# Kernel optimization log

Measured on AMD Instinct MI355X. Metric: run time of the kernel, lower is better.

Reference implementation:

```python
import jax, jax.numpy as jnp
import numpy as np

N_NODES = 100000
N_EDGES = 1600000
N_GRAPHS = 128
CONV = [64, 64, 64]
HID = [256, 128, 2]
GFT = 64
EPS = 1e-5
NEG_SLOPE = 0.01


def leaky_relu(x):
    return jnp.where(x >= 0, x, NEG_SLOPE * x)


def setup_inputs() -> dict:
    key = jax.random.key(0)
    ks = jax.random.split(key, 32)
    inp = {}
    inp['x'] = jax.random.normal(ks[0], (N_NODES, CONV[0]), dtype=jnp.float32)
    inp['edge_index'] = jax.random.randint(ks[1], (2, N_EDGES), 0, N_NODES, dtype=jnp.int64)
    inp['graph_features'] = jax.random.normal(ks[2], (N_GRAPHS, GFT), dtype=jnp.float32)
    inp['batch'] = jnp.sort(jax.random.randint(ks[3], (N_NODES,), 0, N_GRAPHS, dtype=jnp.int64))
    # SAGEConv params per layer: W_l (aggregated branch, with bias), W_r (root branch), BN gamma/beta
    ki = 4
    for li in range(len(CONV) - 1):
        fin, fout = CONV[li], CONV[li + 1]
        s = 1.0 / np.sqrt(fin)
        inp[f'Wl{li}'] = jax.random.uniform(ks[ki], (fin, fout), minval=-s, maxval=s); ki += 1
        inp[f'bl{li}'] = jax.random.uniform(ks[ki], (fout,), minval=-s, maxval=s); ki += 1
        inp[f'Wr{li}'] = jax.random.uniform(ks[ki], (fin, fout), minval=-s, maxval=s); ki += 1
        inp[f'g{li}'] = jnp.ones((fout,), jnp.float32)
        inp[f'b{li}'] = jnp.zeros((fout,), jnp.float32)
    # MLP: Linear(128->256), LeakyReLU, Linear(256->128), LeakyReLU, Linear(128->2)
    dims = [CONV[-1] + GFT] + HID
    for li in range(len(HID)):
        fin, fout = dims[li], dims[li + 1]
        s = 1.0 / np.sqrt(fin)
        inp[f'Wm{li}'] = jax.random.uniform(ks[ki], (fin, fout), minval=-s, maxval=s); ki += 1
        inp[f'bm{li}'] = jax.random.uniform(ks[ki], (fout,), minval=-s, maxval=s); ki += 1
    return inp


def _sage_block(x, src, dst, Wl, bl, Wr, gamma, beta):
    # PyG SAGEConv (aggr='mean'): out = lin_l(mean_{j in N(i)} x_j) + lin_r(x_i)
    msgs = x[src]                                               # [E, Fin] gather
    agg = jax.ops.segment_sum(msgs, dst, num_segments=N_NODES)  # [N, Fin] scatter-add
    deg = jax.ops.segment_sum(jnp.ones((src.shape[0],), x.dtype), dst, num_segments=N_NODES)
    agg = agg / jnp.maximum(deg, 1.0)[:, None]
    h = agg @ Wl + bl + x @ Wr
    h = leaky_relu(h)
    # BatchNorm1d (training mode: batch stats over nodes, biased variance)
    mu = h.mean(axis=0)
    var = h.var(axis=0)
    return (h - mu) * jax.lax.rsqrt(var + EPS) * gamma + beta


def reference(x, edge_index, graph_features, batch,
              Wl0, bl0, Wr0, g0, b0, Wl1, bl1, Wr1, g1, b1,
              Wm0, bm0, Wm1, bm1, Wm2, bm2):
    src, dst = edge_index[0], edge_index[1]
    h = _sage_block(x, src, dst, Wl0, bl0, Wr0, g0, b0)
    h = _sage_block(h, src, dst, Wl1, bl1, Wr1, g1, b1)
    # scatter_mean graph pooling
    pooled = jax.ops.segment_sum(h, batch, num_segments=N_GRAPHS)
    cnt = jax.ops.segment_sum(jnp.ones((h.shape[0],), h.dtype), batch, num_segments=N_GRAPHS)
    pooled = pooled / jnp.maximum(cnt, 1.0)[:, None]
    z = jnp.concatenate([pooled, graph_features], axis=1)       # [G, 128]
    z = leaky_relu(z @ Wm0 + bm0)
    z = leaky_relu(z @ Wm1 + bm1)
    return z @ Wm2 + bm2
```

## Files before the change

kernel.cpp:

```cpp
#include <hip/hip_runtime.h>

#define N_NODES 100000
#define N_EDGES 1600000
#define N_GRAPHS 128
#define FDIM 64
#define EPSV 1e-5f
#define NEG 0.01f

#define NB 782
#define PART_BLOCKS 391
#define NTILES 6250
#define TPB 8
#define GEMM_BLOCKS 782

typedef short bf16x8 __attribute__((ext_vector_type(8)));
typedef float f32x4  __attribute__((ext_vector_type(4)));

__device__ __forceinline__ float leaky(float x){ return x >= 0.f ? x : NEG*x; }

__device__ __forceinline__ unsigned short f2bf(float x){
    unsigned u = __float_as_uint(x);
    return (unsigned short)((u + 0x7fffu + ((u >> 16) & 1u)) >> 16);
}
__device__ __forceinline__ float bf2f(unsigned short b){
    return __uint_as_float(((unsigned)b) << 16);
}

__device__ __forceinline__ void split8(const float4& v0, const float4& v1,
                                       bf16x8& hi, bf16x8& lo){
    float f[8] = {v0.x, v0.y, v0.z, v0.w, v1.x, v1.y, v1.z, v1.w};
    #pragma unroll
    for (int i = 0; i < 8; ++i){
        unsigned u = __float_as_uint(f[i]);
        hi[i] = (short)(u >> 16);
        float lf = f[i] - __uint_as_float(u & 0xffff0000u);
        lo[i] = (short)(__float_as_uint(lf) >> 16);
    }
}

__global__ __launch_bounds__(256) void k_cvt(const float* __restrict__ x,
                                             unsigned short* __restrict__ o){
    int i = blockIdx.x*256 + threadIdx.x;
    if (i < (N_NODES*FDIM)/4){
        float4 v = ((const float4*)x)[i];
        ushort4 r;
        r.x = f2bf(v.x); r.y = f2bf(v.y); r.z = f2bf(v.z); r.w = f2bf(v.w);
        ((ushort4*)o)[i] = r;
    }
}

__global__ __launch_bounds__(256) void k_bh(const int* __restrict__ dst, int* __restrict__ bhist){
    __shared__ int lh[NB];
    int t = threadIdx.x;
    for (int i = t; i < NB; i += 256) lh[i] = 0;
    __syncthreads();
    int base = blockIdx.x * 4096;
    #pragma unroll
    for (int k = 0; k < 16; ++k){
        int e = base + k*256 + t;
        if (e < N_EDGES) atomicAdd(&lh[dst[e] >> 7], 1);
    }
    __syncthreads();
    for (int i = t; i < NB; i += 256) if (lh[i]) atomicAdd(&bhist[i], lh[i]);
}

__global__ __launch_bounds__(256) void k_bscan(const int* __restrict__ bhist,
                                               int* __restrict__ boff, int* __restrict__ cur){
    __shared__ int lds[256];
    int t = threadIdx.x;
    int base = t*4;
    int v0 = (base+0 < NB) ? bhist[base+0] : 0;
    int v1 = (base+1 < NB) ? bhist[base+1] : 0;
    int v2 = (base+2 < NB) ? bhist[base+2] : 0;
    int v3 = (base+3 < NB) ? bhist[base+3] : 0;
    lds[t] = v0+v1+v2+v3; __syncthreads();
    for (int off = 1; off < 256; off <<= 1){
        int add = (t >= off) ? lds[t-off] : 0; __syncthreads();
        lds[t] += add; __syncthreads();
    }
    int excl = (t > 0) ? lds[t-1] : 0;
    int p0 = excl, p1 = excl+v0, p2 = excl+v0+v1, p3 = excl+v0+v1+v2;
    if (base+0 < NB){ boff[base+0] = p0; cur[base+0] = p0; }
    if (base+1 < NB){ boff[base+1] = p1; cur[base+1] = p1; }
    if (base+2 < NB){ boff[base+2] = p2; cur[base+2] = p2; }
    if (base+3 < NB){ boff[base+3] = p3; cur[base+3] = p3; }
    if (t == 0) boff[NB] = N_EDGES;
}

__global__ __launch_bounds__(256) void k_part(const int* __restrict__ src, const int* __restrict__ dst,
                                              int* __restrict__ cur, int* __restrict__ packed){
    __shared__ int lh[NB];
    __shared__ int lc[NB];
    int t = threadIdx.x;
    for (int i = t; i < NB; i += 256) lh[i] = 0;
    __syncthreads();
    int base = blockIdx.x * 4096;
    int d[16];
    #pragma unroll
    for (int k = 0; k < 16; ++k){
        int e = base + k*256 + t;
        d[k] = (e < N_EDGES) ? dst[e] : -1;
        if (d[k] >= 0) atomicAdd(&lh[d[k] >> 7], 1);
    }
    __syncthreads();
    for (int i = t; i < NB; i += 256) lc[i] = atomicAdd(&cur[i], lh[i]);
    __syncthreads();
    #pragma unroll
    for (int k = 0; k < 16; ++k){
        int e = base + k*256 + t;
        if (e < N_EDGES){
            int b = d[k] >> 7;
            int p = atomicAdd(&lc[b], 1);
            packed[p] = (src[e] << 7) | (d[k] & 127);
        }
    }
}

__global__ __launch_bounds__(256) void k_sort(const int* __restrict__ packed,
                                              const int* __restrict__ boff,
                                              int* __restrict__ rs, int* __restrict__ col){
    __shared__ int hist[128];
    __shared__ int curs[128];
    int b = blockIdx.x, t = threadIdx.x;
    int e0 = boff[b], e1 = boff[b+1];
    if (t < 128) hist[t] = 0;
    __syncthreads();
    for (int e = e0 + t; e < e1; e += 256)
        atomicAdd(&hist[packed[e] & 127], 1);
    __syncthreads();
    int cnt = (t < 128) ? hist[t] : 0;
    __syncthreads();
    for (int off = 1; off < 128; off <<= 1){
        int add = (t < 128 && t >= off) ? hist[t-off] : 0;
        __syncthreads();
        if (t < 128) hist[t] += add;
        __syncthreads();
    }
    int nbase = b << 7;
    int nloc = min(128, N_NODES - nbase);
    if (t < nloc){
        int excl = hist[t] - cnt;
        rs[nbase + t] = e0 + excl;
        curs[t] = excl;
    }
    __syncthreads();
    for (int e = e0 + t; e < e1; e += 256){
        int v = packed[e];
        int p = atomicAdd(&curs[v & 127], 1);
        col[e0 + p] = ((unsigned)v) >> 7;
    }
    if (b == 0 && t == 0) rs[N_NODES] = N_EDGES;
}

__global__ __launch_bounds__(256) void k_agg(
    const unsigned short* __restrict__ xin, const int* __restrict__ rs,
    const int* __restrict__ col, float* __restrict__ agg)
{
    int t = threadIdx.x;
    int lane = t & 63;
    int sub = lane >> 4;
    int q   = lane & 15;
    int wid = (blockIdx.x << 2) + (t >> 6);
    const int nw = gridDim.x << 2;
    for (int n = wid; n < N_NODES; n += nw){
        int e0 = __builtin_amdgcn_readfirstlane(rs[n]);
        int e1 = __builtin_amdgcn_readfirstlane(rs[n+1]);
        float ax=0.f, ay=0.f, az=0.f, aw=0.f;
        for (int e = e0; e < e1; e += 16){
            int i0 = e + sub, i1 = e + 4 + sub, i2 = e + 8 + sub, i3 = e + 12 + sub;
            if (i0 < e1){
                uint2 u = ((const uint2*)(xin + ((size_t)col[i0] << 6)))[q];
                ax += __uint_as_float(u.x << 16); ay += __uint_as_float(u.x & 0xffff0000u);
                az += __uint_as_float(u.y << 16); aw += __uint_as_float(u.y & 0xffff0000u);
            }
            if (i1 < e1){
                uint2 u = ((const uint2*)(xin + ((size_t)col[i1] << 6)))[q];
                ax += __uint_as_float(u.x << 16); ay += __uint_as_float(u.x & 0xffff0000u);
                az += __uint_as_float(u.y << 16); aw += __uint_as_float(u.y & 0xffff0000u);
            }
            if (i2 < e1){
                uint2 u = ((const uint2*)(xin + ((size_t)col[i2] << 6)))[q];
                ax += __uint_as_float(u.x << 16); ay += __uint_as_float(u.x & 0xffff0000u);
                az += __uint_as_float(u.y << 16); aw += __uint_as_float(u.y & 0xffff0000u);
            }
            if (i3 < e1){
                uint2 u = ((const uint2*)(xin + ((size_t)col[i3] << 6)))[q];
                ax += __uint_as_float(u.x << 16); ay += __uint_as_float(u.x & 0xffff0000u);
                az += __uint_as_float(u.y << 16); aw += __uint_as_float(u.y & 0xffff0000u);
            }
        }
        ax += __shfl_xor(ax, 16, 64); ay += __shfl_xor(ay, 16, 64);
        az += __shfl_xor(az, 16, 64); aw += __shfl_xor(aw, 16, 64);
        ax += __shfl_xor(ax, 32, 64); ay += __shfl_xor(ay, 32, 64);
        az += __shfl_xor(az, 32, 64); aw += __shfl_xor(aw, 32, 64);
        if (sub == 0){
            float rd = 1.f / fmaxf((float)(e1 - e0), 1.f);
            float4 o = make_float4(ax*rd, ay*rd, az*rd, aw*rd);
            ((float4*)(agg + ((size_t)n << 6)))[q] = o;
        }
    }
}

template<bool AFF, bool XBF>
__global__ __launch_bounds__(256) void k_gemm(
    const float* __restrict__ agg,
    const float* __restrict__ xf, const unsigned short* __restrict__ xbf,
    unsigned short* __restrict__ hout,
    const int* __restrict__ rs, const int* __restrict__ batch,
    const float* __restrict__ Wl, const float* __restrict__ Wr,
    const float* __restrict__ scale,
    const float* __restrict__ bbias, const float* __restrict__ bdelta,
    float* __restrict__ bnpart, float* __restrict__ S)
{
    __shared__ float sS[8*64];
    int t = threadIdx.x;
    int lane = t & 63;
    int jt = t >> 6;
    int g = lane >> 4, r = lane & 15;
    int j = (jt << 4) + r;

    bf16x8 wlh[2], wll[2], wrh[2], wrl[2];
    #pragma unroll
    for (int ks = 0; ks < 2; ++ks){
        #pragma unroll
        for (int i = 0; i < 8; ++i){
            int k = (ks << 5) + (g << 3) + i;
            float s = AFF ? scale[k] : 1.f;
            float wv = Wl[(k << 6) + j] * s;
            unsigned u = __float_as_uint(wv);
            wlh[ks][i] = (short)(u >> 16);
            float lf = wv - __uint_as_float(u & 0xffff0000u);
            wll[ks][i] = (short)(__float_as_uint(lf) >> 16);
            wv = Wr[(k << 6) + j] * s;
            u = __float_as_uint(wv);
            wrh[ks][i] = (short)(u >> 16);
            lf = wv - __uint_as_float(u & 0xffff0000u);
            wrl[ks][i] = (short)(__float_as_uint(lf) >> 16);
        }
    }

    float bb = bbias[j];
    float bd = AFF ? bdelta[j] : 0.f;

    int gbase = 0, span = 0;
    if (AFF){
        for (int i = t; i < 512; i += 256) sS[i] = 0.f;
        int nfirst = blockIdx.x * (TPB*16);
        int nlast  = min(nfirst + TPB*16 - 1, N_NODES - 1);
        gbase = batch[nfirst];
        span  = batch[nlast] - gbase + 1;
        __syncthreads();
    }

    float bs = 0.f, bq = 0.f;
    int c0 = blockIdx.x * TPB;
    int cend = min(c0 + TPB, NTILES);

    auto LOADT = [&](int tile, float4* A, float4* X, bf16x8* XH,
                     int4& R, int& R5, int4& B){
        size_t rowoff = (((size_t)((tile << 4) + r)) << 6) + (g << 3);
        const float4* pa = (const float4*)(agg + rowoff);
        A[0] = pa[0]; A[1] = pa[1]; A[2] = pa[8]; A[3] = pa[9];
        if constexpr (XBF){
            const bf16x8* px = (const bf16x8*)(xbf + rowoff);
            XH[0] = px[0]; XH[1] = px[4];
        } else {
            const float4* px = (const float4*)(xf + rowoff);
            X[0] = px[0]; X[1] = px[1]; X[2] = px[8]; X[3] = px[9];
        }
        if (AFF){
            int nb = (tile << 4) + (g << 2);
            R  = *(const int4*)(rs + nb);
            R5 = rs[nb + 4];
            B  = *(const int4*)(batch + nb);
        }
    };

    auto POOL = [&](int gr, float hv){
        int lg = gr - gbase;
        if (lg < 8) atomicAdd(&sS[(lg << 6) + j], hv);
        else        atomicAdd(&S[(gr << 6) + j], hv);
    };

    auto COMPUTE = [&](int tile, const float4* A, const float4* X, const bf16x8* XH,
                       const int4& R, int R5, const int4& B){
        bf16x8 ah0, al0, ah1, al1;
        split8(A[0], A[1], ah0, al0);
        split8(A[2], A[3], ah1, al1);
        f32x4 accA = {0.f, 0.f, 0.f, 0.f};
        f32x4 accX = {0.f, 0.f, 0.f, 0.f};
        accA = __builtin_amdgcn_mfma_f32_16x16x32_bf16(ah0, wlh[0], accA, 0, 0, 0);
        accA = __builtin_amdgcn_mfma_f32_16x16x32_bf16(ah0, wll[0], accA, 0, 0, 0);
        accA = __builtin_amdgcn_mfma_f32_16x16x32_bf16(al0, wlh[0], accA, 0, 0, 0);
        accA = __builtin_amdgcn_mfma_f32_16x16x32_bf16(ah1, wlh[1], accA, 0, 0, 0);
        accA = __builtin_amdgcn_mfma_f32_16x16x32_bf16(ah1, wll[1], accA, 0, 0, 0);
        accA = __builtin_amdgcn_mfma_f32_16x16x32_bf16(al1, wlh[1], accA, 0, 0, 0);
        if constexpr (XBF){
            accX = __builtin_amdgcn_mfma_f32_16x16x32_bf16(XH[0], wrh[0], accX, 0, 0, 0);
            accX = __builtin_amdgcn_mfma_f32_16x16x32_bf16(XH[0], wrl[0], accX, 0, 0, 0);
            accX = __builtin_amdgcn_mfma_f32_16x16x32_bf16(XH[1], wrh[1], accX, 0, 0, 0);
            accX = __builtin_amdgcn_mfma_f32_16x16x32_bf16(XH[1], wrl[1], accX, 0, 0, 0);
        } else {
            bf16x8 xh0, xl0, xh1, xl1;
            split8(X[0], X[1], xh0, xl0);
            split8(X[2], X[3], xh1, xl1);
            accX = __builtin_amdgcn_mfma_f32_16x16x32_bf16(xh0, wrh[0], accX, 0, 0, 0);
            accX = __builtin_amdgcn_mfma_f32_16x16x32_bf16(xh0, wrl[0], accX, 0, 0, 0);
            accX = __builtin_amdgcn_mfma_f32_16x16x32_bf16(xl0, wrh[0], accX, 0, 0, 0);
            accX = __builtin_amdgcn_mfma_f32_16x16x32_bf16(xh1, wrh[1], accX, 0, 0, 0);
            accX = __builtin_amdgcn_mfma_f32_16x16x32_bf16(xh1, wrl[1], accX, 0, 0, 0);
            accX = __builtin_amdgcn_mfma_f32_16x16x32_bf16(xl1, wrh[1], accX, 0, 0, 0);
        }

        int nb = (tile << 4) + (g << 2);
        if (AFF){
            float hv;
            hv = accA[0] + accX[0] + bb + ((R.y - R.x) > 0 ? bd : 0.f);
            hv = leaky(hv); bs += hv; bq += hv*hv; POOL(B.x, hv);
            hv = accA[1] + accX[1] + bb + ((R.z - R.y) > 0 ? bd : 0.f);
            hv = leaky(hv); bs += hv; bq += hv*hv; POOL(B.y, hv);
            hv = accA[2] + accX[2] + bb + ((R.w - R.z) > 0 ? bd : 0.f);
            hv = leaky(hv); bs += hv; bq += hv*hv; POOL(B.z, hv);
            hv = accA[3] + accX[3] + bb + ((R5 - R.w) > 0 ? bd : 0.f);
            hv = leaky(hv); bs += hv; bq += hv*hv; POOL(B.w, hv);
        } else {
            #pragma unroll
            for (int q = 0; q < 4; ++q){
                float hv = leaky(accA[q] + accX[q] + bb);
                unsigned short h16 = f2bf(hv);
                float hr = bf2f(h16);
                hout[((size_t)(nb + q) << 6) + j] = h16;
                bs += hr; bq += hr*hr;
            }
        }
    };

    float4 Aa[4], Xa[4], Ab[4], Xb[4];
    bf16x8 XHa[2], XHb[2];
    int4 Ra = {0,0,0,0}, Rb = {0,0,0,0}, Ba = {0,0,0,0}, Bb = {0,0,0,0};
    int R5a = 0, R5b = 0;

    LOADT(c0, Aa, Xa, XHa, Ra, R5a, Ba);
    for (int c = c0; c < cend; c += 2){
        if (c + 1 < cend) LOADT(c + 1, Ab, Xb, XHb, Rb, R5b, Bb);
        COMPUTE(c, Aa, Xa, XHa, Ra, R5a, Ba);
        if (c + 2 < cend) LOADT(c + 2, Aa, Xa, XHa, Ra, R5a, Ba);
        if (c + 1 < cend) COMPUTE(c + 1, Ab, Xb, XHb, Rb, R5b, Bb);
    }

    bs += __shfl_xor(bs, 16, 64); bs += __shfl_xor(bs, 32, 64);
    bq += __shfl_xor(bq, 16, 64); bq += __shfl_xor(bq, 32, 64);
    if (lane < 16){
        float* bp = bnpart + ((blockIdx.x & 31) * 128);
        atomicAdd(&bp[(jt << 4) + lane], bs);
        atomicAdd(&bp[64 + (jt << 4) + lane], bq);
    }

    if (AFF){
        __syncthreads();
        int sp = min(span, 8);
        for (int i = t; i < (sp << 6); i += 256){
            float v = sS[i];
            if (v != 0.f) atomicAdd(&S[((gbase + (i >> 6)) << 6) + (i & 63)], v);
        }
    }
}

template<bool FOLD>
__global__ __launch_bounds__(64) void k_bnfin(
    const float* __restrict__ bnpart,
    const float* __restrict__ gamma, const float* __restrict__ beta,
    const float* __restrict__ Wl_nx, const float* __restrict__ Wr_nx,
    const float* __restrict__ bl_nx,
    float* __restrict__ scale, float* __restrict__ shift,
    float* __restrict__ bbias, float* __restrict__ bdelta)
{
    __shared__ float ssh[64];
    int j = threadIdx.x;
    float s = 0.f, q = 0.f;
    #pragma unroll 8
    for (int i = 0; i < 32; ++i){
        s += bnpart[i*128 + j];
        q += bnpart[i*128 + 64 + j];
    }
    float mu  = s * (1.0f/N_NODES);
    float var = q * (1.0f/N_NODES) - mu*mu;
    float sc  = gamma[j] * rsqrtf(var + EPSV);
    float sh  = beta[j] - mu*sc;
    scale[j] = sc; shift[j] = sh;
    if (FOLD){
        ssh[j] = sh;
        __syncthreads();
        float bbv = bl_nx[j], bdv = 0.f;
        #pragma unroll 8
        for (int k = 0; k < 64; ++k){
            bbv += ssh[k] * Wr_nx[(k << 6) + j];
            bdv += ssh[k] * Wl_nx[(k << 6) + j];
        }
        bbias[j] = bbv; bdelta[j] = bdv;
    }
}

__global__ __launch_bounds__(256) void k_mlp(
    const float* __restrict__ S, const int* __restrict__ batch,
    const float* __restrict__ scale, const float* __restrict__ shift,
    const float* __restrict__ gf,
    const float* __restrict__ Wm0, const float* __restrict__ bm0,
    const float* __restrict__ Wm1, const float* __restrict__ bm1,
    const float* __restrict__ Wm2, const float* __restrict__ bm2,
    float* __restrict__ out)
{
    __shared__ int seg[2];
    __shared__ float z[128];
    __shared__ float h1[256];
    __shared__ float h2[128];
    int g = blockIdx.x, t = threadIdx.x;
    if (t < 2){
        int target = g + t;
        int lo = 0, hi = N_NODES;
        while (lo < hi){ int mid = (lo+hi)>>1; if (batch[mid] < target) lo = mid+1; else hi = mid; }
        seg[t] = lo;
    }
    __syncthreads();
    float cnt = (float)(seg[1] - seg[0]);
    if (t < 64)
        z[t] = (scale[t]*S[(g<<6)+t] + cnt*shift[t]) / fmaxf(cnt, 1.f);
    else if (t < 128)
        z[t] = gf[g*64 + (t-64)];
    __syncthreads();
    float acc = bm0[t];
    #pragma unroll 8
    for (int k = 0; k < 128; ++k) acc += z[k]*Wm0[k*256 + t];
    h1[t] = leaky(acc);
    __syncthreads();
    if (t < 128){
        float a = bm1[t];
        #pragma unroll 8
        for (int k = 0; k < 256; ++k) a += h1[k]*Wm1[k*128 + t];
        h2[t] = leaky(a);
    }
    __syncthreads();
    if (t < 2){
        float a = bm2[t];
        for (int k = 0; k < 128; ++k) a += h2[k]*Wm2[k*2 + t];
        out[g*2 + t] = a;
    }
}

extern "C" void kernel_launch(void* const* d_in, const int* in_sizes, int n_in,
                              void* d_out, int out_size, void* d_ws, size_t ws_size,
                              hipStream_t stream) {
    const float* x     = (const float*)d_in[0];
    const int*   ei    = (const int*)d_in[1];
    const float* gf    = (const float*)d_in[2];
    const int*   batch = (const int*)d_in[3];
    const float* Wl0 = (const float*)d_in[4];
    const float* bl0 = (const float*)d_in[5];
    const float* Wr0 = (const float*)d_in[6];
    const float* g0  = (const float*)d_in[7];
    const float* b0  = (const float*)d_in[8];
    const float* Wl1 = (const float*)d_in[9];
    const float* bl1 = (const float*)d_in[10];
    const float* Wr1 = (const float*)d_in[11];
    const float* g1  = (const float*)d_in[12];
    const float* b1  = (const float*)d_in[13];
    const float* Wm0 = (const float*)d_in[14];
    const float* bm0 = (const float*)d_in[15];
    const float* Wm1 = (const float*)d_in[16];
    const float* bm1 = (const float*)d_in[17];
    const float* Wm2 = (const float*)d_in[18];
    const float* bm2 = (const float*)d_in[19];

    int*   bhist  = (int*)d_ws;
    int*   boff   = bhist + NB;
    int*   cur    = boff + NB + 1;
    int*   packed = (int*)d_ws + 2348;
    int*   rs     = packed + N_EDGES;
    int*   col    = rs + 100004;
    unsigned short* xbf  = (unsigned short*)(col + N_EDGES);
    unsigned short* h1bf = xbf + (size_t)N_NODES*FDIM;
    float* bufA   = (float*)(h1bf + (size_t)N_NODES*FDIM);
    float* bnpart = bufA + (size_t)N_NODES*FDIM;
    float* S      = bnpart + 4096;
    float* scale0 = S + N_GRAPHS*FDIM;
    float* shift0 = scale0 + 64;
    float* scale1 = scale0 + 128;
    float* shift1 = scale0 + 192;
    float* bbias  = scale0 + 256;
    float* bdelta = scale0 + 320;

    const int* srcp = ei;
    const int* dstp = ei + N_EDGES;

    hipMemsetAsync(bhist, 0, NB*sizeof(int), stream);
    k_cvt<<<(N_NODES*FDIM/4 + 255)/256, 256, 0, stream>>>(x, xbf);
    k_bh<<<PART_BLOCKS, 256, 0, stream>>>(dstp, bhist);
    k_bscan<<<1, 256, 0, stream>>>(bhist, boff, cur);
    k_part<<<PART_BLOCKS, 256, 0, stream>>>(srcp, dstp, cur, packed);
    k_sort<<<NB, 256, 0, stream>>>(packed, boff, rs, col);

    hipMemsetAsync(bnpart, 0, 4096*sizeof(float), stream);
    k_agg<<<2048, 256, 0, stream>>>(xbf, rs, col, bufA);
    k_gemm<false, false><<<GEMM_BLOCKS, 256, 0, stream>>>(
        bufA, x, nullptr, h1bf, rs, batch,
        Wl0, Wr0, nullptr, bl0, nullptr, bnpart, nullptr);
    k_bnfin<true><<<1, 64, 0, stream>>>(bnpart, g0, b0, Wl1, Wr1, bl1,
                                        scale0, shift0, bbias, bdelta);

    hipMemsetAsync(bnpart, 0, (4096 + N_GRAPHS*FDIM)*sizeof(float), stream);
    k_agg<<<2048, 256, 0, stream>>>(h1bf, rs, col, bufA);
    k_gemm<true, true><<<GEMM_BLOCKS, 256, 0, stream>>>(
        bufA, nullptr, h1bf, nullptr, rs, batch,
        Wl1, Wr1, scale0, bbias, bdelta, bnpart, S);
    k_bnfin<false><<<1, 64, 0, stream>>>(bnpart, g1, b1, nullptr, nullptr, nullptr,
                                         scale1, shift1, nullptr, nullptr);

    k_mlp<<<N_GRAPHS, 256, 0, stream>>>(S, batch, scale1, shift1, gf,
                                        Wm0, bm0, Wm1, bm1, Wm2, bm2, (float*)d_out);
}
```

Before: 300.8 us.

## Fuse neighbor aggregation into the SAGE GEMM kernel via LDS tiles

Replaces the separate aggregation and GEMM kernels with one fused kernel. Each block aggregates 64 nodes into a bf16 LDS tile and then runs the MFMA GEMM directly from LDS. This removes the fp32 agg buffer round trip through global memory and one launch per layer. Layer 0 now uses the bf16 copy of x instead of fp32 with hi/lo splitting, and the aggregated input loses its low-precision correction term, trading accuracy for fewer MFMAs. The software pipelining of tile loads is dropped, and per-block occupancy changes with the LDS tile.

New measurement: 368.6 us. 22.6% more time.

```diff
diff --git a/kernel.cpp b/kernel.cpp
--- a/kernel.cpp
+++ b/kernel.cpp
@@ -9,9 +9,7 @@
 
 #define NB 782
 #define PART_BLOCKS 391
-#define NTILES 6250
-#define TPB 8
-#define GEMM_BLOCKS 782
+#define FUSED_BLOCKS 1563
 
 typedef short bf16x8 __attribute__((ext_vector_type(8)));
 typedef float f32x4  __attribute__((ext_vector_type(4)));
@@ -24,18 +22,6 @@
 }
 __device__ __forceinline__ float bf2f(unsigned short b){
     return __uint_as_float(((unsigned)b) << 16);
-}
-
-__device__ __forceinline__ void split8(const float4& v0, const float4& v1,
-                                       bf16x8& hi, bf16x8& lo){
-    float f[8] = {v0.x, v0.y, v0.z, v0.w, v1.x, v1.y, v1.z, v1.w};
-    #pragma unroll
-    for (int i = 0; i < 8; ++i){
-        unsigned u = __float_as_uint(f[i]);
-        hi[i] = (short)(u >> 16);
-        float lf = f[i] - __uint_as_float(u & 0xffff0000u);
-        lo[i] = (short)(__float_as_uint(lf) >> 16);
-    }
 }
 
 __global__ __launch_bounds__(256) void k_cvt(const float* __restrict__ x,
@@ -152,72 +138,25 @@
     if (b == 0 && t == 0) rs[N_NODES] = N_EDGES;
 }
 
-__global__ __launch_bounds__(256) void k_agg(
-    const unsigned short* __restrict__ xin, const int* __restrict__ rs,
-    const int* __restrict__ col, float* __restrict__ agg)
-{
-    int t = threadIdx.x;
-    int lane = t & 63;
-    int sub = lane >> 4;
-    int q   = lane & 15;
-    int wid = (blockIdx.x << 2) + (t >> 6);
-    const int nw = gridDim.x << 2;
-    for (int n = wid; n < N_NODES; n += nw){
-        int e0 = __builtin_amdgcn_readfirstlane(rs[n]);
-        int e1 = __builtin_amdgcn_readfirstlane(rs[n+1]);
-        float ax=0.f, ay=0.f, az=0.f, aw=0.f;
-        for (int e = e0; e < e1; e += 16){
-            int i0 = e + sub, i1 = e + 4 + sub, i2 = e + 8 + sub, i3 = e + 12 + sub;
-            if (i0 < e1){
-                uint2 u = ((const uint2*)(xin + ((size_t)col[i0] << 6)))[q];
-                ax += __uint_as_float(u.x << 16); ay += __uint_as_float(u.x & 0xffff0000u);
-                az += __uint_as_float(u.y << 16); aw += __uint_as_float(u.y & 0xffff0000u);
-            }
-            if (i1 < e1){
-                uint2 u = ((const uint2*)(xin + ((size_t)col[i1] << 6)))[q];
-                ax += __uint_as_float(u.x << 16); ay += __uint_as_float(u.x & 0xffff0000u);
-                az += __uint_as_float(u.y << 16); aw += __uint_as_float(u.y & 0xffff0000u);
-            }
-            if (i2 < e1){
-                uint2 u = ((const uint2*)(xin + ((size_t)col[i2] << 6)))[q];
-                ax += __uint_as_float(u.x << 16); ay += __uint_as_float(u.x & 0xffff0000u);
-                az += __uint_as_float(u.y << 16); aw += __uint_as_float(u.y & 0xffff0000u);
-            }
-            if (i3 < e1){
-                uint2 u = ((const uint2*)(xin + ((size_t)col[i3] << 6)))[q];
-                ax += __uint_as_float(u.x << 16); ay += __uint_as_float(u.x & 0xffff0000u);
-                az += __uint_as_float(u.y << 16); aw += __uint_as_float(u.y & 0xffff0000u);
-            }
-        }
-        ax += __shfl_xor(ax, 16, 64); ay += __shfl_xor(ay, 16, 64);
-        az += __shfl_xor(az, 16, 64); aw += __shfl_xor(aw, 16, 64);
-        ax += __shfl_xor(ax, 32, 64); ay += __shfl_xor(ay, 32, 64);
-        az += __shfl_xor(az, 32, 64); aw += __shfl_xor(aw, 32, 64);
-        if (sub == 0){
-            float rd = 1.f / fmaxf((float)(e1 - e0), 1.f);
-            float4 o = make_float4(ax*rd, ay*rd, az*rd, aw*rd);
-            ((float4*)(agg + ((size_t)n << 6)))[q] = o;
-        }
-    }
-}
-
-template<bool AFF, bool XBF>
-__global__ __launch_bounds__(256) void k_gemm(
-    const float* __restrict__ agg,
-    const float* __restrict__ xf, const unsigned short* __restrict__ xbf,
+template<bool AFF>
+__global__ __launch_bounds__(256) void k_fused(
+    const unsigned short* __restrict__ xbf,
     unsigned short* __restrict__ hout,
-    const int* __restrict__ rs, const int* __restrict__ batch,
+    const int* __restrict__ rs, const int* __restrict__ col,
+    const int* __restrict__ batch,
     const float* __restrict__ Wl, const float* __restrict__ Wr,
     const float* __restrict__ scale,
     const float* __restrict__ bbias, const float* __restrict__ bdelta,
     float* __restrict__ bnpart, float* __restrict__ S)
 {
+    __shared__ unsigned short lA[64*72];
     __shared__ float sS[8*64];
     int t = threadIdx.x;
     int lane = t & 63;
-    int jt = t >> 6;
+    int w = t >> 6;
     int g = lane >> 4, r = lane & 15;
-    int j = (jt << 4) + r;
+    int j = (w << 4) + r;
+    int nbase = blockIdx.x << 6;
 
     bf16x8 wlh[2], wll[2], wrh[2], wrl[2];
     #pragma unroll
@@ -245,84 +184,95 @@
     int gbase = 0, span = 0;
     if (AFF){
         for (int i = t; i < 512; i += 256) sS[i] = 0.f;
-        int nfirst = blockIdx.x * (TPB*16);
-        int nlast  = min(nfirst + TPB*16 - 1, N_NODES - 1);
-        gbase = batch[nfirst];
-        span  = batch[nlast] - gbase + 1;
-        __syncthreads();
-    }
+        gbase = batch[nbase];
+        int nlast = min(nbase + 63, N_NODES - 1);
+        span = batch[nlast] - gbase + 1;
+    }
+
+    #pragma unroll 1
+    for (int i = 0; i < 16; ++i){
+        int n = nbase + (w << 4) + i;
+        if (n < N_NODES){
+            int e0 = __builtin_amdgcn_readfirstlane(rs[n]);
+            int e1 = __builtin_amdgcn_readfirstlane(rs[n+1]);
+            float ax=0.f, ay=0.f, az=0.f, aw=0.f;
+            for (int e = e0; e < e1; e += 16){
+                int i0 = e + g, i1 = e + 4 + g, i2 = e + 8 + g, i3 = e + 12 + g;
+                if (i0 < e1){
+                    uint2 u = ((const uint2*)(xbf + ((size_t)col[i0] << 6)))[r];
+                    ax += __uint_as_float(u.x << 16); ay += __uint_as_float(u.x & 0xffff0000u);
+                    az += __uint_as_float(u.y << 16); aw += __uint_as_float(u.y & 0xffff0000u);
+                }
+                if (i1 < e1){
+                    uint2 u = ((const uint2*)(xbf + ((size_t)col[i1] << 6)))[r];
+                    ax += __uint_as_float(u.x << 16); ay += __uint_as_float(u.x & 0xffff0000u);
+                    az += __uint_as_float(u.y << 16); aw += __uint_as_float(u.y & 0xffff0000u);
+                }
+                if (i2 < e1){
+                    uint2 u = ((const uint2*)(xbf + ((size_t)col[i2] << 6)))[r];
+                    ax += __uint_as_float(u.x << 16); ay += __uint_as_float(u.x & 0xffff0000u);
+                    az += __uint_as_float(u.y << 16); aw += __uint_as_float(u.y & 0xffff0000u);
+                }
+                if (i3 < e1){
+                    uint2 u = ((const uint2*)(xbf + ((size_t)col[i3] << 6)))[r];
+                    ax += __uint_as_float(u.x << 16); ay += __uint_as_float(u.x & 0xffff0000u);
+                    az += __uint_as_float(u.y << 16); aw += __uint_as_float(u.y & 0xffff0000u);
+                }
+            }
+            ax += __shfl_xor(ax, 16, 64); ay += __shfl_xor(ay, 16, 64);
+            az += __shfl_xor(az, 16, 64); aw += __shfl_xor(aw, 16, 64);
+            ax += __shfl_xor(ax, 32, 64); ay += __shfl_xor(ay, 32, 64);
+            az += __shfl_xor(az, 32, 64); aw += __shfl_xor(aw, 32, 64);
+            if (g == 0){
+                float rd = 1.f / fmaxf((float)(e1 - e0), 1.f);
+                ushort4 o;
+                o.x = f2bf(ax*rd); o.y = f2bf(ay*rd);
+                o.z = f2bf(az*rd); o.w = f2bf(aw*rd);
+                *(ushort4*)&lA[((w << 4) + i)*72 + (r << 2)] = o;
+            }
+        }
+    }
+    __syncthreads();
 
     float bs = 0.f, bq = 0.f;
-    int c0 = blockIdx.x * TPB;
-    int cend = min(c0 + TPB, NTILES);
-
-    auto LOADT = [&](int tile, float4* A, float4* X, bf16x8* XH,
-                     int4& R, int& R5, int4& B){
-        size_t rowoff = (((size_t)((tile << 4) + r)) << 6) + (g << 3);
-        const float4* pa = (const float4*)(agg + rowoff);
-        A[0] = pa[0]; A[1] = pa[1]; A[2] = pa[8]; A[3] = pa[9];
-        if constexpr (XBF){
-            const bf16x8* px = (const bf16x8*)(xbf + rowoff);
-            XH[0] = px[0]; XH[1] = px[4];
-        } else {
-            const float4* px = (const float4*)(xf + rowoff);
-            X[0] = px[0]; X[1] = px[1]; X[2] = px[8]; X[3] = px[9];
-        }
-        if (AFF){
-            int nb = (tile << 4) + (g << 2);
-            R  = *(const int4*)(rs + nb);
-            R5 = rs[nb + 4];
-            B  = *(const int4*)(batch + nb);
-        }
-    };
-
-    auto POOL = [&](int gr, float hv){
-        int lg = gr - gbase;
-        if (lg < 8) atomicAdd(&sS[(lg << 6) + j], hv);
-        else        atomicAdd(&S[(gr << 6) + j], hv);
-    };
-
-    auto COMPUTE = [&](int tile, const float4* A, const float4* X, const bf16x8* XH,
-                       const int4& R, int R5, const int4& B){
-        bf16x8 ah0, al0, ah1, al1;
-        split8(A[0], A[1], ah0, al0);
-        split8(A[2], A[3], ah1, al1);
+    #pragma unroll 1
+    for (int nt = 0; nt < 4; ++nt){
+        int trow = nbase + (nt << 4);
+        if (trow >= N_NODES) break;
+        bf16x8 a0 = *(const bf16x8*)&lA[((nt << 4) + r)*72 + (g << 3)];
+        bf16x8 a1 = *(const bf16x8*)&lA[((nt << 4) + r)*72 + 32 + (g << 3)];
+        const bf16x8* px = (const bf16x8*)(xbf + (((size_t)(trow + r)) << 6) + (g << 3));
+        bf16x8 x0 = px[0], x1 = px[4];
+
         f32x4 accA = {0.f, 0.f, 0.f, 0.f};
         f32x4 accX = {0.f, 0.f, 0.f, 0.f};
-        accA = __builtin_amdgcn_mfma_f32_16x16x32_bf16(ah0, wlh[0], accA, 0, 0, 0);
-        accA = __builtin_amdgcn_mfma_f32_16x16x32_bf16(ah0, wll[0], accA, 0, 0, 0);
-        accA = __builtin_amdgcn_mfma_f32_16x16x32_bf16(al0, wlh[0], accA, 0, 0, 0);
-        accA = __builtin_amdgcn_mfma_f32_16x16x32_bf16(ah1, wlh[1], accA, 0, 0, 0);
-        accA = __builtin_amdgcn_mfma_f32_16x16x32_bf16(ah1, wll[1], accA, 0, 0, 0);
-        accA = __builtin_amdgcn_mfma_f32_16x16x32_bf16(al1, wlh[1], accA, 0, 0, 0);
-        if constexpr (XBF){
-            accX = __builtin_amdgcn_mfma_f32_16x16x32_bf16(XH[0], wrh[0], accX, 0, 0, 0);
-            accX = __builtin_amdgcn_mfma_f32_16x16x32_bf16(XH[0], wrl[0], accX, 0, 0, 0);
-            accX = __builtin_amdgcn_mfma_f32_16x16x32_bf16(XH[1], wrh[1], accX, 0, 0, 0);
-            accX = __builtin_amdgcn_mfma_f32_16x16x32_bf16(XH[1], wrl[1], accX, 0, 0, 0);
-        } else {
-            bf16x8 xh0, xl0, xh1, xl1;
-            split8(X[0], X[1], xh0, xl0);
-            split8(X[2], X[3], xh1, xl1);
-            accX = __builtin_amdgcn_mfma_f32_16x16x32_bf16(xh0, wrh[0], accX, 0, 0, 0);
-            accX = __builtin_amdgcn_mfma_f32_16x16x32_bf16(xh0, wrl[0], accX, 0, 0, 0);
-            accX = __builtin_amdgcn_mfma_f32_16x16x32_bf16(xl0, wrh[0], accX, 0, 0, 0);
-            accX = __builtin_amdgcn_mfma_f32_16x16x32_bf16(xh1, wrh[1], accX, 0, 0, 0);
-            accX = __builtin_amdgcn_mfma_f32_16x16x32_bf16(xh1, wrl[1], accX, 0, 0, 0);
-            accX = __builtin_amdgcn_mfma_f32_16x16x32_bf16(xl1, wrh[1], accX, 0, 0, 0);
-        }
-
-        int nb = (tile << 4) + (g << 2);
+        accA = __builtin_amdgcn_mfma_f32_16x16x32_bf16(a0, wlh[0], accA, 0, 0, 0);
+        accA = __builtin_amdgcn_mfma_f32_16x16x32_bf16(a0, wll[0], accA, 0, 0, 0);
+        accA = __builtin_amdgcn_mfma_f32_16x16x32_bf16(a1, wlh[1], accA, 0, 0, 0);
+        accA = __builtin_amdgcn_mfma_f32_16x16x32_bf16(a1, wll[1], accA, 0, 0, 0);
+        accX = __builtin_amdgcn_mfma_f32_16x16x32_bf16(x0, wrh[0], accX, 0, 0, 0);
+        accX = __builtin_amdgcn_mfma_f32_16x16x32_bf16(x0, wrl[0], accX, 0, 0, 0);
+        accX = __builtin_amdgcn_mfma_f32_16x16x32_bf16(x1, wrh[1], accX, 0, 0, 0);
+        accX = __builtin_amdgcn_mfma_f32_16x16x32_bf16(x1, wrl[1], accX, 0, 0, 0);
+
+        int nb = trow + (g << 2);
         if (AFF){
+            int4 R = *(const int4*)(rs + nb);
+            int  R5 = rs[nb + 4];
+            int4 B = *(const int4*)(batch + nb);
             float hv;
             hv = accA[0] + accX[0] + bb + ((R.y - R.x) > 0 ? bd : 0.f);
-            hv = leaky(hv); bs += hv; bq += hv*hv; POOL(B.x, hv);
+            hv = leaky(hv); bs += hv; bq += hv*hv;
+            { int lg = B.x - gbase; if (lg < 8) atomicAdd(&sS[(lg<<6)+j], hv); else atomicAdd(&S[(B.x<<6)+j], hv); }
             hv = accA[1] + accX[1] + bb + ((R.z - R.y) > 0 ? bd : 0.f);
-            hv = leaky(hv); bs += hv; bq += hv*hv; POOL(B.y, hv);
+            hv = leaky(hv); bs += hv; bq += hv*hv;
+            { int lg = B.y - gbase; if (lg < 8) atomicAdd(&sS[(lg<<6)+j], hv); else atomicAdd(&S[(B.y<<6)+j], hv); }
             hv = accA[2] + accX[2] + bb + ((R.w - R.z) > 0 ? bd : 0.f);
-            hv = leaky(hv); bs += hv; bq += hv*hv; POOL(B.z, hv);
+            hv = leaky(hv); bs += hv; bq += hv*hv;
+            { int lg = B.z - gbase; if (lg < 8) atomicAdd(&sS[(lg<<6)+j], hv); else atomicAdd(&S[(B.z<<6)+j], hv); }
             hv = accA[3] + accX[3] + bb + ((R5 - R.w) > 0 ? bd : 0.f);
-            hv = leaky(hv); bs += hv; bq += hv*hv; POOL(B.w, hv);
+            hv = leaky(hv); bs += hv; bq += hv*hv;
+            { int lg = B.w - gbase; if (lg < 8) atomicAdd(&sS[(lg<<6)+j], hv); else atomicAdd(&S[(B.w<<6)+j], hv); }
         } else {
             #pragma unroll
             for (int q = 0; q < 4; ++q){
@@ -333,27 +283,14 @@
                 bs += hr; bq += hr*hr;
             }
         }
-    };
-
-    float4 Aa[4], Xa[4], Ab[4], Xb[4];
-    bf16x8 XHa[2], XHb[2];
-    int4 Ra = {0,0,0,0}, Rb = {0,0,0,0}, Ba = {0,0,0,0}, Bb = {0,0,0,0};
-    int R5a = 0, R5b = 0;
-
-    LOADT(c0, Aa, Xa, XHa, Ra, R5a, Ba);
-    for (int c = c0; c < cend; c += 2){
-        if (c + 1 < cend) LOADT(c + 1, Ab, Xb, XHb, Rb, R5b, Bb);
-        COMPUTE(c, Aa, Xa, XHa, Ra, R5a, Ba);
-        if (c + 2 < cend) LOADT(c + 2, Aa, Xa, XHa, Ra, R5a, Ba);
-        if (c + 1 < cend) COMPUTE(c + 1, Ab, Xb, XHb, Rb, R5b, Bb);
     }
 
     bs += __shfl_xor(bs, 16, 64); bs += __shfl_xor(bs, 32, 64);
     bq += __shfl_xor(bq, 16, 64); bq += __shfl_xor(bq, 32, 64);
     if (lane < 16){
         float* bp = bnpart + ((blockIdx.x & 31) * 128);
-        atomicAdd(&bp[(jt << 4) + lane], bs);
-        atomicAdd(&bp[64 + (jt << 4) + lane], bq);
+        atomicAdd(&bp[(w << 4) + lane], bs);
+        atomicAdd(&bp[64 + (w << 4) + lane], bq);
     }
 
     if (AFF){
@@ -479,8 +416,7 @@
     int*   col    = rs + 100004;
     unsigned short* xbf  = (unsigned short*)(col + N_EDGES);
     unsigned short* h1bf = xbf + (size_t)N_NODES*FDIM;
-    float* bufA   = (float*)(h1bf + (size_t)N_NODES*FDIM);
-    float* bnpart = bufA + (size_t)N_NODES*FDIM;
+    float* bnpart = (float*)(h1bf + (size_t)N_NODES*FDIM);
     float* S      = bnpart + 4096;
     float* scale0 = S + N_GRAPHS*FDIM;
     float* shift0 = scale0 + 64;
@@ -500,17 +436,15 @@
     k_sort<<<NB, 256, 0, stream>>>(packed, boff, rs, col);
 
     hipMemsetAsync(bnpart, 0, 4096*sizeof(float), stream);
-    k_agg<<<2048, 256, 0, stream>>>(xbf, rs, col, bufA);
-    k_gemm<false, false><<<GEMM_BLOCKS, 256, 0, stream>>>(
-        bufA, x, nullptr, h1bf, rs, batch,
+    k_fused<false><<<FUSED_BLOCKS, 256, 0, stream>>>(
+        xbf, h1bf, rs, col, batch,
         Wl0, Wr0, nullptr, bl0, nullptr, bnpart, nullptr);
     k_bnfin<true><<<1, 64, 0, stream>>>(bnpart, g0, b0, Wl1, Wr1, bl1,
                                         scale0, shift0, bbias, bdelta);
 
     hipMemsetAsync(bnpart, 0, (4096 + N_GRAPHS*FDIM)*sizeof(float), stream);
-    k_agg<<<2048, 256, 0, stream>>>(h1bf, rs, col, bufA);
-    k_gemm<true, true><<<GEMM_BLOCKS, 256, 0, stream>>>(
-        bufA, nullptr, h1bf, nullptr, rs, batch,
+    k_fused<true><<<FUSED_BLOCKS, 256, 0, stream>>>(
+        h1bf, nullptr, rs, col, batch,
         Wl1, Wr1, scale0, bbias, bdelta, bnpart, S);
     k_bnfin<false><<<1, 64, 0, stream>>>(bnpart, g1, b1, nullptr, nullptr, nullptr,
                                          scale1, shift1, nullptr, nullptr);
```
